# Kernel tuning notes

Hardware: AMD Instinct MI355X
Metric: run time of the kernel (lower is better)

## Reference

```python
import jax, jax.numpy as jnp
import numpy as np
from jax import lax

L, H, C, V, BLK = 6, 12, 768, 50257, 1024
B, T = 4, 1024
HD = C // H
EPS = 1e-5


def _norm(key, shape, scale=0.02):
    return jax.random.normal(key, shape, dtype=jnp.float32) * scale


def setup_inputs() -> dict:
    key = jax.random.key(0)
    ks = jax.random.split(key, 16)
    idx = jax.random.randint(ks[0], (B, T), 0, V)
    inp = {
        "idx": idx,
        "wte": _norm(ks[1], (V, C)),
        "wpe": _norm(ks[2], (BLK, C)),
        "ln1_s": jnp.ones((L, C)),
        "ln1_b": jnp.zeros((L, C)),
        "qkv_w": _norm(ks[3], (L, C, 3 * C)),
        "qkv_b": jnp.zeros((L, 3 * C)),
        "proj_w": _norm(ks[4], (L, C, C)),
        "proj_b": jnp.zeros((L, C)),
        "ln2_s": jnp.ones((L, C)),
        "ln2_b": jnp.zeros((L, C)),
        "fc_w": _norm(ks[5], (L, C, 4 * C)),
        "fc_b": jnp.zeros((L, 4 * C)),
        "fcp_w": _norm(ks[6], (L, 4 * C, C)),
        "fcp_b": jnp.zeros((L, C)),
        "lnf_s": jnp.ones((C,)),
        "lnf_b": jnp.zeros((C,)),
    }
    return inp


def layer_norm(x, s, b):
    mu = jnp.mean(x, axis=-1, keepdims=True)
    var = jnp.mean(jnp.square(x - mu), axis=-1, keepdims=True)
    return (x - mu) * lax.rsqrt(var + EPS) * s + b


def block(x, p):
    ln1_s, ln1_b, qkv_w, qkv_b, proj_w, proj_b, ln2_s, ln2_b, fc_w, fc_b, fcp_w, fcp_b = p
    Bx, Tx, Cx = x.shape
    h = layer_norm(x, ln1_s, ln1_b)
    qkv = h @ qkv_w + qkv_b  # [B,T,3C]
    q, k, v = jnp.split(qkv, 3, axis=-1)
    q = q.reshape(Bx, Tx, H, HD).swapaxes(1, 2)  # [B,H,T,hd]
    k = k.reshape(Bx, Tx, H, HD).swapaxes(1, 2)
    v = v.reshape(Bx, Tx, H, HD).swapaxes(1, 2)
    attn = jnp.einsum("bhqd,bhkd->bhqk", q, k) / jnp.sqrt(jnp.float32(HD))
    mask = jnp.tril(jnp.ones((Tx, Tx), dtype=bool))
    attn = jnp.where(mask, attn, -jnp.inf)
    attn = jax.nn.softmax(attn, axis=-1)
    y = jnp.einsum("bhqk,bhkd->bhqd", attn, v)
    y = y.swapaxes(1, 2).reshape(Bx, Tx, Cx)
    x = x + (y @ proj_w + proj_b)
    h = layer_norm(x, ln2_s, ln2_b)
    h = jax.nn.gelu(h @ fc_w + fc_b, approximate=True)
    x = x + (h @ fcp_w + fcp_b)
    return x


def reference(idx, wte, wpe, ln1_s, ln1_b, qkv_w, qkv_b, proj_w, proj_b,
              ln2_s, ln2_b, fc_w, fc_b, fcp_w, fcp_b, lnf_s, lnf_b):
    Tx = idx.shape[1]
    x = wte[idx] + wpe[:Tx][None]  # [B,T,C]
    params = (ln1_s, ln1_b, qkv_w, qkv_b, proj_w, proj_b,
              ln2_s, ln2_b, fc_w, fc_b, fcp_w, fcp_b)
    def step(carry, p):
        return block(carry, p), None
    x, _ = lax.scan(step, x, params)
    x = layer_norm(x, lnf_s, lnf_b)
    logits = x @ wte.T  # tied embedding attend
    return logits
```

## Files before the change

### kernel.cpp

```cpp
#include <hip/hip_runtime.h>
#include <math.h>

#define LNUM 6
#define HNUM 12
#define CDIM 768
#define VDIM 50257
#define BDIM 4
#define TDIM 1024
#define NTOK 4096

typedef __bf16 bf16;
typedef __bf16 bf16x8 __attribute__((ext_vector_type(8)));
typedef float  floatx4 __attribute__((ext_vector_type(4)));
typedef unsigned int u32;

__device__ inline void gload16(const bf16* gsrc, bf16* lds) {
  __builtin_amdgcn_global_load_lds(
      (const __attribute__((address_space(1))) u32*)gsrc,
      (__attribute__((address_space(3))) u32*)lds, 16, 0, 0);
}

__global__ void k_cvt_bf16(const float* __restrict__ in, bf16* __restrict__ out, long n) {
  long i = ((long)blockIdx.x * blockDim.x + threadIdx.x) * 4;
  long stride = (long)gridDim.x * blockDim.x * 4;
  for (; i < n; i += stride) {
    float4 v = *reinterpret_cast<const float4*>(in + i);
    bf16 b0 = (bf16)v.x, b1 = (bf16)v.y, b2 = (bf16)v.z, b3 = (bf16)v.w;
    ushort4 pk;
    pk.x = __builtin_bit_cast(unsigned short, b0);
    pk.y = __builtin_bit_cast(unsigned short, b1);
    pk.z = __builtin_bit_cast(unsigned short, b2);
    pk.w = __builtin_bit_cast(unsigned short, b3);
    *reinterpret_cast<ushort4*>(out + i) = pk;
  }
}

#define TILES_QKV  1728
#define TILES_PROJ 576
#define TILES_FC   2304
#define TILES_FCP  2304
#define TILES_LAYER (TILES_QKV + TILES_PROJ + TILES_FC + TILES_FCP)

__global__ __launch_bounds__(256) void k_trans_all(
    const float* __restrict__ qkv_w, const float* __restrict__ proj_w,
    const float* __restrict__ fc_w, const float* __restrict__ fcp_w,
    bf16* __restrict__ wq, bf16* __restrict__ wp,
    bf16* __restrict__ wf, bf16* __restrict__ wfp) {
  __shared__ float tile[32][33];
  int bid = blockIdx.x;
  int layer = bid / TILES_LAYER, r = bid % TILES_LAYER;
  const float* src; bf16* dst; int K, N, tx, ty;
  if (r < TILES_QKV) {
    src = qkv_w + (size_t)layer * CDIM * 3 * CDIM; dst = wq + (size_t)layer * CDIM * 3 * CDIM;
    K = CDIM; N = 3 * CDIM; tx = r % 72; ty = r / 72;
  } else if (r < TILES_QKV + TILES_PROJ) {
    r -= TILES_QKV;
    src = proj_w + (size_t)layer * CDIM * CDIM; dst = wp + (size_t)layer * CDIM * CDIM;
    K = CDIM; N = CDIM; tx = r % 24; ty = r / 24;
  } else if (r < TILES_QKV + TILES_PROJ + TILES_FC) {
    r -= TILES_QKV + TILES_PROJ;
    src = fc_w + (size_t)layer * CDIM * 4 * CDIM; dst = wf + (size_t)layer * CDIM * 4 * CDIM;
    K = CDIM; N = 4 * CDIM; tx = r % 96; ty = r / 96;
  } else {
    r -= TILES_QKV + TILES_PROJ + TILES_FC;
    src = fcp_w + (size_t)layer * 4 * CDIM * CDIM; dst = wfp + (size_t)layer * 4 * CDIM * CDIM;
    K = 4 * CDIM; N = CDIM; tx = r % 24; ty = r / 24;
  }
  int n0 = tx * 32, k0 = ty * 32;
  int nx = threadIdx.x & 31, tyy = threadIdx.x >> 5;
  #pragma unroll
  for (int p = 0; p < 4; ++p) {
    int k = tyy + p * 8;
    tile[k][nx] = src[(size_t)(k0 + k) * N + n0 + nx];
  }
  __syncthreads();
  #pragma unroll
  for (int p = 0; p < 4; ++p) {
    int n = tyy + p * 8;
    dst[(size_t)(n0 + n) * K + k0 + nx] = (bf16)tile[nx][n];
  }
}

__global__ void k_embed(const int* __restrict__ idx, const float* __restrict__ wte,
                        const float* __restrict__ wpe, float* __restrict__ x) {
  int tok = blockIdx.x;
  int t = tok & (TDIM - 1);
  int id = idx[tok];
  const float* a = wte + (size_t)id * CDIM;
  const float* p = wpe + (size_t)t * CDIM;
  float* o = x + (size_t)tok * CDIM;
  for (int c = threadIdx.x; c < CDIM; c += 256) o[c] = a[c] + p[c];
}

__global__ __launch_bounds__(256) void k_layernorm(const float* __restrict__ x,
    const float* __restrict__ sc, const float* __restrict__ bi, bf16* __restrict__ out) {
  __shared__ float red[8];
  int row = blockIdx.x;
  const float* xr = x + (size_t)row * CDIM;
  int t = threadIdx.x;
  float v0 = xr[t], v1 = xr[t + 256], v2 = xr[t + 512];
  float s = v0 + v1 + v2;
  #pragma unroll
  for (int o = 32; o > 0; o >>= 1) s += __shfl_down(s, o);
  if ((t & 63) == 0) red[t >> 6] = s;
  __syncthreads();
  float mean = (red[0] + red[1] + red[2] + red[3]) * (1.0f / CDIM);
  float d0 = v0 - mean, d1 = v1 - mean, d2 = v2 - mean;
  float q = d0 * d0 + d1 * d1 + d2 * d2;
  #pragma unroll
  for (int o = 32; o > 0; o >>= 1) q += __shfl_down(q, o);
  if ((t & 63) == 0) red[4 + (t >> 6)] = q;
  __syncthreads();
  float var = (red[4] + red[5] + red[6] + red[7]) * (1.0f / CDIM);
  float rs = rsqrtf(var + 1e-5f);
  bf16* orow = out + (size_t)row * CDIM;
  orow[t]       = (bf16)(d0 * rs * sc[t]       + bi[t]);
  orow[t + 256] = (bf16)(d1 * rs * sc[t + 256] + bi[t + 256]);
  orow[t + 512] = (bf16)(d2 * rs * sc[t + 512] + bi[t + 512]);
}

__device__ inline float gelu_f(float x) {
  float x3 = x * x * x;
  return 0.5f * x * (1.0f + tanhf(0.7978845608028654f * (x + 0.044715f * x3)));
}

__global__ __launch_bounds__(512, 1) void k_gemm_logits(
    const bf16* __restrict__ A, const bf16* __restrict__ Bt,
    float* __restrict__ Cf, int N, int K) {
  __shared__ __align__(16) bf16 smem[7 * 8192];
  bf16* Bs = smem;
  bf16* As = smem + 4 * 8192;
  const int nwg = gridDim.x;
  const int id = blockIdx.x;
  const int swz = (id & 7) * (nwg >> 3) + (id >> 3);
  const int m0 = (swz & 15) * 256;
  const int n0 = (swz >> 4) * 256;
  const int tid = threadIdx.x, lane = tid & 63, wave = tid >> 6;
  const int wr = wave >> 2, wc = wave & 3;
  const int g = lane >> 4, r16 = lane & 15;
  const int numK = K >> 5;
  const int wsl = wave * 512;

  const int srow = wave * 16 + (lane >> 2);
  const int scol = ((lane & 3) ^ ((lane >> 3) & 3)) * 8;
  const bf16* at  = A  + (size_t)(m0 + srow) * K + scol;
  const bf16* at1 = A  + (size_t)(m0 + srow + 128) * K + scol;
  const bf16* bt  = Bt + (size_t)(n0 + srow) * K + scol;
  const bf16* bt1 = Bt + (size_t)(n0 + srow + 128) * K + scol;
  const int sw = (g ^ ((r16 >> 1) & 3)) * 8;
  const int a_off = (wr * 128 + r16) * 32 + sw;
  const int b_off = (wc * 64 + r16) * 32 + sw;

  floatx4 acc[8][4] = {};

#define STBd(s0, s1, pb) do { gload16((s0), Bs + (pb) * 8192 + wsl); \
                              gload16((s1), Bs + (pb) * 8192 + wsl + 4096); } while (0)
#define STAd(s0, s1, pb) do { gload16((s0), As + (pb) * 8192 + wsl); \
                              gload16((s1), As + (pb) * 8192 + wsl + 4096); } while (0)

  STBd(bt,      bt1,      0);
  STAd(at,      at1,      0);
  STBd(bt + 32, bt1 + 32, 1);
  STAd(at + 32, at1 + 32, 1);
  STBd(bt + 64, bt1 + 64, 2);
  asm volatile("s_waitcnt vmcnt(6)" ::: "memory");
  __builtin_amdgcn_s_barrier();

  for (int t = 0; t < numK; ++t) {
    const int ab = t % 3, bb = t & 3;
    bf16x8 af[4], bfr[4];

    #pragma unroll
    for (int j = 0; j < 4; ++j) bfr[j] = *(const bf16x8*)&Bs[bb * 8192 + b_off + j * 512];
    #pragma unroll
    for (int i = 0; i < 4; ++i) af[i] = *(const bf16x8*)&As[ab * 8192 + a_off + i * 512];
    if (t + 2 < numK) STAd(at + 64, at1 + 64, (t + 2) % 3);
    __builtin_amdgcn_s_barrier();
    asm volatile("s_waitcnt lgkmcnt(0)" ::: "memory");
    __builtin_amdgcn_s_setprio(1);
    #pragma unroll
    for (int i = 0; i < 4; ++i)
      #pragma unroll
      for (int j = 0; j < 4; ++j)
        acc[i][j] = __builtin_amdgcn_mfma_f32_16x16x32_bf16(af[i], bfr[j], acc[i][j], 0, 0, 0);
    __builtin_amdgcn_s_setprio(0);
    __builtin_amdgcn_s_barrier();

    #pragma unroll
    for (int i = 0; i < 4; ++i) af[i] = *(const bf16x8*)&As[ab * 8192 + a_off + (i + 4) * 512];
    if (t + 3 < numK) STBd(bt + 96, bt1 + 96, (t + 3) & 3);
    __builtin_amdgcn_s_barrier();
    asm volatile("s_waitcnt lgkmcnt(0)" ::: "memory");
    __builtin_amdgcn_s_setprio(1);
    #pragma unroll
    for (int i = 0; i < 4; ++i)
      #pragma unroll
      for (int j = 0; j < 4; ++j)
        acc[i + 4][j] = __builtin_amdgcn_mfma_f32_16x16x32_bf16(af[i], bfr[j], acc[i + 4][j], 0, 0, 0);
    __builtin_amdgcn_s_setprio(0);
    if (t + 3 < numK)      { asm volatile("s_waitcnt vmcnt(6)" ::: "memory"); }
    else if (t + 2 < numK) { asm volatile("s_waitcnt vmcnt(4)" ::: "memory"); }
    else                   { asm volatile("s_waitcnt vmcnt(0)" ::: "memory"); }
    __builtin_amdgcn_s_barrier();

    at += 32; at1 += 32; bt += 32; bt1 += 32;
  }
#undef STBd
#undef STAd

  float* sb = reinterpret_cast<float*>(smem) + wave * 1088;
  const int seg = lane & 15, rq = lane >> 4;
  const int mrow_base = m0 + wr * 128;
  const int ncol_base = n0 + wc * 64;
  #pragma unroll
  for (int mf = 0; mf < 8; ++mf) {
    #pragma unroll
    for (int nf = 0; nf < 4; ++nf) {
      #pragma unroll
      for (int q = 0; q < 4; ++q)
        sb[(g * 4 + q) * 68 + nf * 16 + r16] = acc[mf][nf][q];
    }
    #pragma unroll
    for (int pz = 0; pz < 4; ++pz) {
      int row = rq + pz * 4;
      floatx4 v = *reinterpret_cast<const floatx4*>(&sb[row * 68 + seg * 4]);
      int m = mrow_base + mf * 16 + row;
      int n = ncol_base + seg * 4;
      if (n + 4 <= N) {
        __builtin_nontemporal_store(v, reinterpret_cast<floatx4*>(&Cf[(size_t)m * N + n]));
      } else {
        #pragma unroll
        for (int e = 0; e < 4; ++e)
          if (n + e < N) Cf[(size_t)m * N + n + e] = v[e];
      }
    }
  }
}

template<int TBM, int EPI>
__global__ __launch_bounds__(512, 1) void k_gemm8(
    const bf16* __restrict__ A, const bf16* __restrict__ Bt,
    const float* __restrict__ bias,
    float* __restrict__ Cf, bf16* __restrict__ Cb,
    int N, int K) {
  constexpr int MI = TBM / 32;
  constexpr int MH = MI / 2;
  constexpr int MTILES = 4096 / TBM;
  __shared__ __align__(16) bf16 smem[2 * 8192 + 2 * TBM * 32];
  bf16* Bs = smem;
  bf16* As = smem + 2 * 8192;
  const int nwg = gridDim.x;
  const int id = blockIdx.x;
  const int swz = (id & 7) * (nwg >> 3) + (id >> 3);
  const int m0 = (swz % MTILES) * TBM;
  const int n0 = (swz / MTILES) * 256;
  const int tid = threadIdx.x, lane = tid & 63, wave = tid >> 6;
  const int wr = wave >> 2, wc = wave & 3;
  const int g = lane >> 4, r16 = lane & 15;
  const int numK = K >> 5;
  const int wsl = wave * 512;

  const int srow = wave * 16 + (lane >> 2);
  const int scol = ((lane & 3) ^ ((lane >> 3) & 3)) * 8;
  const bf16* at  = A  + (size_t)(m0 + srow) * K + scol;
  const bf16* at1 = A  + (size_t)(m0 + srow + 128) * K + scol;
  const bf16* bt  = Bt + (size_t)(n0 + srow) * K + scol;
  const bf16* bt1 = Bt + (size_t)(n0 + srow + 128) * K + scol;
  const int sw = (g ^ ((r16 >> 1) & 3)) * 8;
  const int a_off = (wr * (TBM / 2) + r16) * 32 + sw;
  const int b_off = (wc * 64 + r16) * 32 + sw;

  floatx4 acc[MI][4] = {};

#define STB(s0, s1, pb) do { gload16((s0), Bs + (pb) * 8192 + wsl); \
                             gload16((s1), Bs + (pb) * 8192 + wsl + 4096); } while (0)
#define STA(s0, s1, pb) do { gload16((s0), As + (pb) * TBM * 32 + wsl); \
                             if constexpr (TBM == 256) gload16((s1), As + (pb) * TBM * 32 + wsl + 4096); } while (0)

  STB(bt, bt1, 0);
  STA(at, at1, 0);
  STB(bt + 32, bt1 + 32, 1);
  asm volatile("s_waitcnt vmcnt(2)" ::: "memory");
  __builtin_amdgcn_s_barrier();

  for (int t = 0; t < numK; ++t) {
    const int p = t & 1, pn = p ^ 1;
    bf16x8 af[MH], bfr[4];

    #pragma unroll
    for (int j = 0; j < 4; ++j) bfr[j] = *(const bf16x8*)&Bs[p * 8192 + b_off + j * 512];
    #pragma unroll
    for (int i = 0; i < MH; ++i) af[i] = *(const bf16x8*)&As[p * TBM * 32 + a_off + i * 512];
    if (t + 1 < numK) STA(at + 32, at1 + 32, pn);
    __builtin_amdgcn_s_barrier();
    asm volatile("s_waitcnt lgkmcnt(0)" ::: "memory");
    __builtin_amdgcn_s_setprio(1);
    #pragma unroll
    for (int i = 0; i < MH; ++i)
      #pragma unroll
      for (int j = 0; j < 4; ++j)
        acc[i][j] = __builtin_amdgcn_mfma_f32_16x16x32_bf16(af[i], bfr[j], acc[i][j], 0, 0, 0);
    __builtin_amdgcn_s_setprio(0);
    __builtin_amdgcn_s_barrier();

    #pragma unroll
    for (int i = 0; i < MH; ++i) af[i] = *(const bf16x8*)&As[p * TBM * 32 + a_off + (i + MH) * 512];
    if (t + 2 < numK) STB(bt + 64, bt1 + 64, p);
    __builtin_amdgcn_s_barrier();
    asm volatile("s_waitcnt lgkmcnt(0)" ::: "memory");
    __builtin_amdgcn_s_setprio(1);
    #pragma unroll
    for (int i = 0; i < MH; ++i)
      #pragma unroll
      for (int j = 0; j < 4; ++j)
        acc[i + MH][j] = __builtin_amdgcn_mfma_f32_16x16x32_bf16(af[i], bfr[j], acc[i + MH][j], 0, 0, 0);
    __builtin_amdgcn_s_setprio(0);
    if (t + 2 < numK) { asm volatile("s_waitcnt vmcnt(2)" ::: "memory"); }
    else              { asm volatile("s_waitcnt vmcnt(0)" ::: "memory"); }
    __builtin_amdgcn_s_barrier();

    at += 32; at1 += 32; bt += 32; bt1 += 32;
  }
#undef STB
#undef STA

  bf16* sb = smem + wave * 1152;
  const int rr_rd = lane & 15, seg = lane >> 4;
  const int nb = n0 + wc * 64 + r16;
  float bv[4];
  #pragma unroll
  for (int j = 0; j < 4; ++j) bv[j] = bias[nb + j * 16];
  #pragma unroll
  for (int mf = 0; mf < MI; ++mf) {
    #pragma unroll
    for (int j = 0; j < 4; ++j) {
      #pragma unroll
      for (int q = 0; q < 4; ++q) {
        float v = acc[mf][j][q] + bv[j];
        if (EPI == 3) v = gelu_f(v);
        sb[(g * 4 + q) * 72 + j * 16 + r16] = (bf16)v;
      }
    }
    bf16x8 o0 = *(const bf16x8*)&sb[rr_rd * 72 + seg * 16];
    bf16x8 o1 = *(const bf16x8*)&sb[rr_rd * 72 + seg * 16 + 8];
    size_t orow = (size_t)(m0 + wr * (TBM / 2) + mf * 16 + rr_rd) * N + (n0 + wc * 64 + seg * 16);
    *(bf16x8*)&Cb[orow] = o0;
    *(bf16x8*)&Cb[orow + 8] = o1;
  }
}

template<int TBM, int MI, int NI, int EPI>
__global__ __launch_bounds__(256) void k_gemm(
    const bf16* __restrict__ A, const bf16* __restrict__ Bt,
    const float* __restrict__ bias, const float* __restrict__ resid,
    float* __restrict__ Cf, bf16* __restrict__ Cb,
    int M, int N, int K) {
  constexpr int BN = 128;
  constexpr int WGN = BN / (NI * 16);
  constexpr int AI = TBM / 32;
  constexpr int BI = BN / 32;
  __shared__ __align__(16) bf16 As[TBM * 64];
  __shared__ __align__(16) bf16 Bs[BN * 64];
  const int m0 = blockIdx.x * TBM, n0 = blockIdx.y * BN;
  const int tid = threadIdx.x;
  const int lane = tid & 63, wave = tid >> 6;
  const int wr = wave / WGN, wc = wave % WGN;
  const int l8 = lane >> 3, s8 = lane & 7;
  const int g = lane >> 4, r16 = lane & 15;

  floatx4 acc[MI][NI] = {};

  const bf16* a_src = A + (size_t)(m0 + l8) * K + s8 * 8;
  const bf16* b_src = Bt + (size_t)(n0 + l8) * K + s8 * 8;

  for (int k0 = 0; k0 < K; k0 += 64) {
    #pragma unroll
    for (int t = 0; t < AI; ++t) {
      int row0 = wave * (TBM / 4) + t * 8;
      gload16(a_src + (size_t)row0 * K + k0, &As[row0 * 64]);
    }
    #pragma unroll
    for (int t = 0; t < BI; ++t) {
      int row0 = wave * 32 + t * 8;
      gload16(b_src + (size_t)row0 * K + k0, &Bs[row0 * 64]);
    }
    __syncthreads();
    #pragma unroll
    for (int kk = 0; kk < 2; ++kk) {
      bf16x8 af[MI], bfr[NI];
      #pragma unroll
      for (int i = 0; i < MI; ++i)
        af[i] = *reinterpret_cast<const bf16x8*>(&As[(wr * MI * 16 + i * 16 + r16) * 64 + g * 8 + kk * 32]);
      #pragma unroll
      for (int j = 0; j < NI; ++j)
        bfr[j] = *reinterpret_cast<const bf16x8*>(&Bs[(wc * NI * 16 + j * 16 + r16) * 64 + g * 8 + kk * 32]);
      #pragma unroll
      for (int i = 0; i < MI; ++i) {
        #pragma unroll
        for (int j = 0; j < NI; ++j)
          acc[i][j] = __builtin_amdgcn_mfma_f32_16x16x32_bf16(af[i], bfr[j], acc[i][j], 0, 0, 0);
      }
    }
    __syncthreads();
  }

  int mb = m0 + wr * MI * 16 + g * 4;
  int nb = n0 + wc * NI * 16 + r16;
  #pragma unroll
  for (int j = 0; j < NI; ++j) {
    int n = nb + j * 16;
    if (n >= N) continue;
    float bv = (EPI >= 2) ? bias[n] : 0.0f;
    #pragma unroll
    for (int i = 0; i < MI; ++i) {
      #pragma unroll
      for (int q = 0; q < 4; ++q) {
        int m = mb + i * 16 + q;
        float v = acc[i][j][q] + bv;
        size_t o = (size_t)m * N + n;
        if (EPI == 2)      Cf[o] = v + resid[o];
        else if (EPI == 3) Cb[o] = (bf16)gelu_f(v);
        else if (EPI == 4) Cb[o] = (bf16)v;
        else               Cf[o] = v;
      }
    }
  }
}

__global__ __launch_bounds__(256) void k_vtrans(const bf16* __restrict__ qkv, bf16* __restrict__ vt) {
  __shared__ bf16 tile[64][72];
  int bh = blockIdx.x, t0 = blockIdx.y * 64;
  int b = bh / HNUM, h = bh % HNUM;
  int tid = threadIdx.x;
  int r8 = tid >> 3, s8 = tid & 7;
  #pragma unroll
  for (int p = 0; p < 2; ++p) {
    int row = p * 32 + r8;
    uint4 v = *reinterpret_cast<const uint4*>(
        qkv + (size_t)(b * TDIM + t0 + row) * (3 * CDIM) + 2 * CDIM + h * 64 + s8 * 8);
    *reinterpret_cast<uint4*>(&tile[row][s8 * 8]) = v;
  }
  __syncthreads();
  int d = tid >> 2, q4 = tid & 3;
  #pragma unroll
  for (int half = 0; half < 2; ++half) {
    int t = q4 * 16 + half * 8;
    bf16x8 o;
    #pragma unroll
    for (int u = 0; u < 8; ++u) o[u] = tile[t + u][d];
    *reinterpret_cast<bf16x8*>(vt + (size_t)bh * (64 * TDIM) + (size_t)d * TDIM + t0 + t) = o;
  }
}

__global__ __launch_bounds__(256) void k_attn(const bf16* __restrict__ qkv,
                                              const bf16* __restrict__ vt,
                                              bf16* __restrict__ y) {
  __shared__ __align__(16) bf16 Ks[64 * 64];
  __shared__ __align__(16) bf16 Vs[64 * 64];
  __shared__ __align__(16) bf16 Ps[64 * 64];
  const int bh = blockIdx.x, qt = blockIdx.y;
  const int b = bh / HNUM, h = bh % HNUM;
  const int tid = threadIdx.x, lane = tid & 63, wave = tid >> 6;
  const int g = lane >> 4, r16 = lane & 15;
  const int w16 = wave * 16;
  const int r8 = tid >> 3, s8 = tid & 7;

  bf16x8 qf[2];
  {
    const bf16* qsrc = qkv + (size_t)(b * TDIM + qt * 64 + w16 + r16) * (3 * CDIM) + h * 64 + g * 8;
    qf[0] = *reinterpret_cast<const bf16x8*>(qsrc);
    qf[1] = *reinterpret_cast<const bf16x8*>(qsrc + 32);
  }

  float m_r[4], l_r[4];
  floatx4 yacc[4] = {};
  #pragma unroll
  for (int q = 0; q < 4; ++q) { m_r[q] = -1e30f; l_r[q] = 0.f; }

  for (int kt = 0; kt <= qt; ++kt) {
    __syncthreads();
    #pragma unroll
    for (int p = 0; p < 2; ++p) {
      int row = p * 32 + r8;
      uint4 kv = *reinterpret_cast<const uint4*>(
          qkv + (size_t)(b * TDIM + kt * 64 + row) * (3 * CDIM) + CDIM + h * 64 + s8 * 8);
      *reinterpret_cast<uint4*>(&Ks[row * 64 + ((s8 ^ (row & 7)) * 8)]) = kv;
      uint4 vv = *reinterpret_cast<const uint4*>(
          vt + (size_t)bh * (64 * TDIM) + (size_t)row * TDIM + kt * 64 + s8 * 8);
      *reinterpret_cast<uint4*>(&Vs[row * 64 + ((s8 ^ (row & 7)) * 8)]) = vv;
    }
    __syncthreads();

    floatx4 sa[4] = {};
    #pragma unroll
    for (int c = 0; c < 2; ++c) {
      bf16x8 kf[4];
      #pragma unroll
      for (int j = 0; j < 4; ++j) {
        int krow = j * 16 + r16;
        kf[j] = *reinterpret_cast<const bf16x8*>(&Ks[krow * 64 + (((g + 4 * c) ^ (krow & 7)) * 8)]);
      }
      #pragma unroll
      for (int j = 0; j < 4; ++j)
        sa[j] = __builtin_amdgcn_mfma_f32_16x16x32_bf16(qf[c], kf[j], sa[j], 0, 0, 0);
    }

    const bool diag = (kt == qt);
    float p_v[4][4];
    #pragma unroll
    for (int q = 0; q < 4; ++q) {
      int qrow = w16 + g * 4 + q;
      float mx = -1e30f;
      #pragma unroll
      for (int j = 0; j < 4; ++j) {
        float s = sa[j][q] * 0.125f;
        if (diag && (r16 + j * 16) > qrow) s = -1e30f;
        p_v[j][q] = s;
        mx = fmaxf(mx, s);
      }
      #pragma unroll
      for (int o = 1; o < 16; o <<= 1) mx = fmaxf(mx, __shfl_xor(mx, o));
      float mnew = fmaxf(m_r[q], mx);
      float ps = 0.f;
      #pragma unroll
      for (int j = 0; j < 4; ++j) {
        float p = __expf(p_v[j][q] - mnew);
        p_v[j][q] = p;
        ps += p;
      }
      #pragma unroll
      for (int o = 1; o < 16; o <<= 1) ps += __shfl_xor(ps, o);
      float alpha = __expf(m_r[q] - mnew);
      m_r[q] = mnew;
      l_r[q] = l_r[q] * alpha + ps;
      #pragma unroll
      for (int j = 0; j < 4; ++j) yacc[j][q] *= alpha;
      #pragma unroll
      for (int j = 0; j < 4; ++j) {
        int col = r16 + j * 16;
        Ps[qrow * 64 + (col ^ ((qrow & 7) << 3))] = (bf16)p_v[j][q];
      }
    }

    #pragma unroll
    for (int ks = 0; ks < 2; ++ks) {
      int prow = w16 + r16;
      bf16x8 pa = *reinterpret_cast<const bf16x8*>(&Ps[prow * 64 + (((g + 4 * ks) ^ (prow & 7)) * 8)]);
      #pragma unroll
      for (int j = 0; j < 4; ++j) {
        int vrow = j * 16 + r16;
        bf16x8 vb = *reinterpret_cast<const bf16x8*>(&Vs[vrow * 64 + (((g + 4 * ks) ^ (vrow & 7)) * 8)]);
        yacc[j] = __builtin_amdgcn_mfma_f32_16x16x32_bf16(pa, vb, yacc[j], 0, 0, 0);
      }
    }
  }

  #pragma unroll
  for (int q = 0; q < 4; ++q) {
    float inv = 1.0f / l_r[q];
    int tok = b * TDIM + qt * 64 + w16 + g * 4 + q;
    #pragma unroll
    for (int j = 0; j < 4; ++j)
      y[(size_t)tok * CDIM + h * 64 + r16 + j * 16] = (bf16)(yacc[j][q] * inv);
  }
}

extern "C" void kernel_launch(void* const* d_in, const int* in_sizes, int n_in,
                              void* d_out, int out_size, void* d_ws, size_t ws_size,
                              hipStream_t stream) {
  (void)in_sizes; (void)n_in; (void)out_size;
  const int*   idx    = (const int*)  d_in[0];
  const float* wte    = (const float*)d_in[1];
  const float* wpe    = (const float*)d_in[2];
  const float* ln1_s  = (const float*)d_in[3];
  const float* ln1_b  = (const float*)d_in[4];
  const float* qkv_w  = (const float*)d_in[5];
  const float* qkv_b  = (const float*)d_in[6];
  const float* proj_w = (const float*)d_in[7];
  const float* proj_b = (const float*)d_in[8];
  const float* ln2_s  = (const float*)d_in[9];
  const float* ln2_b  = (const float*)d_in[10];
  const float* fc_w   = (const float*)d_in[11];
  const float* fc_b   = (const float*)d_in[12];
  const float* fcp_w  = (const float*)d_in[13];
  const float* fcp_b  = (const float*)d_in[14];
  const float* lnf_s  = (const float*)d_in[15];
  const float* lnf_b  = (const float*)d_in[16];
  float* logits = (float*)d_out;

  char* base = (char*)d_ws;
  size_t off = 0;
  auto alloc = [&](size_t bytes) -> void* {
    void* p = base + off;
    off += (bytes + 255) & ~(size_t)255;
    return p;
  };
  bf16*  wte_bf  = (bf16*) alloc((size_t)VDIM * CDIM * 2);
  bf16*  wq_all  = (bf16*) alloc((size_t)LNUM * 3 * CDIM * CDIM * 2);
  bf16*  wp_all  = (bf16*) alloc((size_t)LNUM * CDIM * CDIM * 2);
  bf16*  wf_all  = (bf16*) alloc((size_t)LNUM * 4 * CDIM * CDIM * 2);
  bf16*  wfp_all = (bf16*) alloc((size_t)LNUM * 4 * CDIM * CDIM * 2);
  float* x       = (float*)alloc((size_t)NTOK * CDIM * 4);
  bf16*  hb      = (bf16*) alloc((size_t)NTOK * CDIM * 2);
  bf16*  qkv_bf  = (bf16*) alloc((size_t)NTOK * 3 * CDIM * 2);
  bf16*  vt      = (bf16*) alloc((size_t)BDIM * HNUM * 64 * TDIM * 2);
  bf16*  yb      = (bf16*) alloc((size_t)NTOK * CDIM * 2);
  bf16*  gb      = (bf16*) alloc((size_t)NTOK * 4 * CDIM * 2);
  if (off > ws_size) return;

  k_cvt_bf16<<<4096, 256, 0, stream>>>(wte, wte_bf, (long)VDIM * CDIM);
  k_trans_all<<<LNUM * TILES_LAYER, 256, 0, stream>>>(qkv_w, proj_w, fc_w, fcp_w,
                                                      wq_all, wp_all, wf_all, wfp_all);
  k_embed<<<NTOK, 256, 0, stream>>>(idx, wte, wpe, x);

  for (int l = 0; l < LNUM; ++l) {
    const bf16* wq  = wq_all  + (size_t)l * 3 * CDIM * CDIM;
    const bf16* wp  = wp_all  + (size_t)l * CDIM * CDIM;
    const bf16* wf  = wf_all  + (size_t)l * 4 * CDIM * CDIM;
    const bf16* wfp = wfp_all + (size_t)l * 4 * CDIM * CDIM;

    k_layernorm<<<NTOK, 256, 0, stream>>>(x, ln1_s + l*CDIM, ln1_b + l*CDIM, hb);
    k_gemm8<128,4><<<32 * 9, 512, 0, stream>>>(hb, wq, qkv_b + (size_t)l*3*CDIM, nullptr, qkv_bf, 3*CDIM, CDIM);
    k_vtrans<<<dim3(BDIM*HNUM, TDIM/64), 256, 0, stream>>>(qkv_bf, vt);
    k_attn<<<dim3(BDIM*HNUM, TDIM/64), 256, 0, stream>>>(qkv_bf, vt, yb);
    k_gemm<64,4,2,2><<<dim3(NTOK/64, 6), 256, 0, stream>>>(yb, wp, proj_b + (size_t)l*CDIM, x, x, nullptr, NTOK, CDIM, CDIM);
    k_layernorm<<<NTOK, 256, 0, stream>>>(x, ln2_s + l*CDIM, ln2_b + l*CDIM, hb);
    k_gemm8<128,3><<<32 * 12, 512, 0, stream>>>(hb, wf, fc_b + (size_t)l*4*CDIM, nullptr, gb, 4*CDIM, CDIM);
    k_gemm<64,4,2,2><<<dim3(NTOK/64, 6), 256, 0, stream>>>(gb, wfp, fcp_b + (size_t)l*CDIM, x, x, nullptr, NTOK, CDIM, 4*CDIM);
  }

  k_layernorm<<<NTOK, 256, 0, stream>>>(x, lnf_s, lnf_b, hb);
  int ntile = (VDIM + 255) / 256;
  k_gemm_logits<<<16 * ntile, 512, 0, stream>>>(hb, wte_bf, logits, VDIM, CDIM);
}
```

Before: 1.827 ms.

## Pipeline projection GEMMs with double-buffered LDS and widen attention tiles to 128 queries

Replaces the generic 64x128 projection/FC-proj GEMM with a 128x128 kernel that double-buffers A and B tiles in swizzled LDS, splits each K-step into two MFMA phases with barriers and priority hints, and adds an XCD-aware block swizzle. Attention now handles 128 query rows per block with 8 waves sharing each K/V tile, so K/V loads are amortized over more queries, and waves past the causal limit skip compute. The logits store also changes from a nontemporal store to a plain memcpy store. The cost is fewer workgroups (192 for the projections) and some idle waves on diagonal attention tiles.

```diff
diff --git a/kernel.cpp b/kernel.cpp
--- a/kernel.cpp
+++ b/kernel.cpp
@@ -227,7 +227,7 @@
       int m = mrow_base + mf * 16 + row;
       int n = ncol_base + seg * 4;
       if (n + 4 <= N) {
-        __builtin_nontemporal_store(v, reinterpret_cast<floatx4*>(&Cf[(size_t)m * N + n]));
+        __builtin_memcpy(&Cf[(size_t)m * N + n], &v, 16);
       } else {
         #pragma unroll
         for (int e = 0; e < 4; ++e)
@@ -349,79 +349,101 @@
   }
 }
 
-template<int TBM, int MI, int NI, int EPI>
-__global__ __launch_bounds__(256) void k_gemm(
+__global__ __launch_bounds__(256, 1) void k_gemmp(
     const bf16* __restrict__ A, const bf16* __restrict__ Bt,
-    const float* __restrict__ bias, const float* __restrict__ resid,
-    float* __restrict__ Cf, bf16* __restrict__ Cb,
-    int M, int N, int K) {
-  constexpr int BN = 128;
-  constexpr int WGN = BN / (NI * 16);
-  constexpr int AI = TBM / 32;
-  constexpr int BI = BN / 32;
-  __shared__ __align__(16) bf16 As[TBM * 64];
-  __shared__ __align__(16) bf16 Bs[BN * 64];
-  const int m0 = blockIdx.x * TBM, n0 = blockIdx.y * BN;
-  const int tid = threadIdx.x;
-  const int lane = tid & 63, wave = tid >> 6;
-  const int wr = wave / WGN, wc = wave % WGN;
-  const int l8 = lane >> 3, s8 = lane & 7;
+    const float* __restrict__ bias, float* __restrict__ Cf,
+    int N, int K) {
+  __shared__ __align__(16) bf16 smem[4 * 4096];
+  bf16* Bs = smem;
+  bf16* As = smem + 2 * 4096;
+  const int nwg = gridDim.x;
+  const int id = blockIdx.x;
+  const int swz = (id & 7) * (nwg >> 3) + (id >> 3);
+  const int m0 = (swz & 31) * 128;
+  const int n0 = (swz >> 5) * 128;
+  const int tid = threadIdx.x, lane = tid & 63, wave = tid >> 6;
+  const int wr = wave >> 1, wc = wave & 1;
   const int g = lane >> 4, r16 = lane & 15;
-
-  floatx4 acc[MI][NI] = {};
-
-  const bf16* a_src = A + (size_t)(m0 + l8) * K + s8 * 8;
-  const bf16* b_src = Bt + (size_t)(n0 + l8) * K + s8 * 8;
-
-  for (int k0 = 0; k0 < K; k0 += 64) {
-    #pragma unroll
-    for (int t = 0; t < AI; ++t) {
-      int row0 = wave * (TBM / 4) + t * 8;
-      gload16(a_src + (size_t)row0 * K + k0, &As[row0 * 64]);
-    }
-    #pragma unroll
-    for (int t = 0; t < BI; ++t) {
-      int row0 = wave * 32 + t * 8;
-      gload16(b_src + (size_t)row0 * K + k0, &Bs[row0 * 64]);
-    }
-    __syncthreads();
-    #pragma unroll
-    for (int kk = 0; kk < 2; ++kk) {
-      bf16x8 af[MI], bfr[NI];
-      #pragma unroll
-      for (int i = 0; i < MI; ++i)
-        af[i] = *reinterpret_cast<const bf16x8*>(&As[(wr * MI * 16 + i * 16 + r16) * 64 + g * 8 + kk * 32]);
-      #pragma unroll
-      for (int j = 0; j < NI; ++j)
-        bfr[j] = *reinterpret_cast<const bf16x8*>(&Bs[(wc * NI * 16 + j * 16 + r16) * 64 + g * 8 + kk * 32]);
-      #pragma unroll
-      for (int i = 0; i < MI; ++i) {
-        #pragma unroll
-        for (int j = 0; j < NI; ++j)
-          acc[i][j] = __builtin_amdgcn_mfma_f32_16x16x32_bf16(af[i], bfr[j], acc[i][j], 0, 0, 0);
-      }
-    }
-    __syncthreads();
-  }
-
-  int mb = m0 + wr * MI * 16 + g * 4;
-  int nb = n0 + wc * NI * 16 + r16;
-  #pragma unroll
-  for (int j = 0; j < NI; ++j) {
+  const int numK = K >> 5;
+  const int wsl = wave * 512;
+
+  const int srow = wave * 16 + (lane >> 2);
+  const int scol = ((lane & 3) ^ ((lane >> 3) & 3)) * 8;
+  const bf16* at  = A  + (size_t)(m0 + srow) * K + scol;
+  const bf16* at1 = A  + (size_t)(m0 + srow + 64) * K + scol;
+  const bf16* bt  = Bt + (size_t)(n0 + srow) * K + scol;
+  const bf16* bt1 = Bt + (size_t)(n0 + srow + 64) * K + scol;
+  const int sw = (g ^ ((r16 >> 1) & 3)) * 8;
+  const int a_off = (wr * 64 + r16) * 32 + sw;
+  const int b_off = (wc * 64 + r16) * 32 + sw;
+
+  floatx4 acc[4][4] = {};
+
+#define STBp(s0, s1, pb) do { gload16((s0), Bs + (pb) * 4096 + wsl); \
+                              gload16((s1), Bs + (pb) * 4096 + 2048 + wsl); } while (0)
+#define STAp(s0, s1, pb) do { gload16((s0), As + (pb) * 4096 + wsl); \
+                              gload16((s1), As + (pb) * 4096 + 2048 + wsl); } while (0)
+
+  STBp(bt, bt1, 0);
+  STAp(at, at1, 0);
+  STBp(bt + 32, bt1 + 32, 1);
+  asm volatile("s_waitcnt vmcnt(2)" ::: "memory");
+  __builtin_amdgcn_s_barrier();
+
+  for (int t = 0; t < numK; ++t) {
+    const int p = t & 1, pn = p ^ 1;
+    bf16x8 af[2], bfr[4];
+
+    #pragma unroll
+    for (int j = 0; j < 4; ++j) bfr[j] = *(const bf16x8*)&Bs[p * 4096 + b_off + j * 512];
+    #pragma unroll
+    for (int i = 0; i < 2; ++i) af[i] = *(const bf16x8*)&As[p * 4096 + a_off + i * 512];
+    if (t + 1 < numK) STAp(at + 32, at1 + 32, pn);
+    __builtin_amdgcn_s_barrier();
+    asm volatile("s_waitcnt lgkmcnt(0)" ::: "memory");
+    __builtin_amdgcn_s_setprio(1);
+    #pragma unroll
+    for (int i = 0; i < 2; ++i)
+      #pragma unroll
+      for (int j = 0; j < 4; ++j)
+        acc[i][j] = __builtin_amdgcn_mfma_f32_16x16x32_bf16(af[i], bfr[j], acc[i][j], 0, 0, 0);
+    __builtin_amdgcn_s_setprio(0);
+    __builtin_amdgcn_s_barrier();
+
+    #pragma unroll
+    for (int i = 0; i < 2; ++i) af[i] = *(const bf16x8*)&As[p * 4096 + a_off + (i + 2) * 512];
+    if (t + 2 < numK) STBp(bt + 64, bt1 + 64, p);
+    __builtin_amdgcn_s_barrier();
+    asm volatile("s_waitcnt lgkmcnt(0)" ::: "memory");
+    __builtin_amdgcn_s_setprio(1);
+    #pragma unroll
+    for (int i = 0; i < 2; ++i)
+      #pragma unroll
+      for (int j = 0; j < 4; ++j)
+        acc[i + 2][j] = __builtin_amdgcn_mfma_f32_16x16x32_bf16(af[i], bfr[j], acc[i + 2][j], 0, 0, 0);
+    __builtin_amdgcn_s_setprio(0);
+    if (t + 2 < numK) { asm volatile("s_waitcnt vmcnt(2)" ::: "memory"); }
+    else              { asm volatile("s_waitcnt vmcnt(0)" ::: "memory"); }
+    __builtin_amdgcn_s_barrier();
+
+    at += 32; at1 += 32; bt += 32; bt1 += 32;
+  }
+#undef STBp
+#undef STAp
+
+  const int mb = m0 + wr * 64 + g * 4;
+  const int nb = n0 + wc * 64 + r16;
+  #pragma unroll
+  for (int j = 0; j < 4; ++j) {
     int n = nb + j * 16;
-    if (n >= N) continue;
-    float bv = (EPI >= 2) ? bias[n] : 0.0f;
-    #pragma unroll
-    for (int i = 0; i < MI; ++i) {
+    float bv = bias[n];
+    #pragma unroll
+    for (int i = 0; i < 4; ++i) {
       #pragma unroll
       for (int q = 0; q < 4; ++q) {
         int m = mb + i * 16 + q;
-        float v = acc[i][j][q] + bv;
         size_t o = (size_t)m * N + n;
-        if (EPI == 2)      Cf[o] = v + resid[o];
-        else if (EPI == 3) Cb[o] = (bf16)gelu_f(v);
-        else if (EPI == 4) Cb[o] = (bf16)v;
-        else               Cf[o] = v;
+        Cf[o] = Cf[o] + acc[i][j][q] + bv;
       }
     }
   }
@@ -452,22 +474,23 @@
   }
 }
 
-__global__ __launch_bounds__(256) void k_attn(const bf16* __restrict__ qkv,
+__global__ __launch_bounds__(512) void k_attn(const bf16* __restrict__ qkv,
                                               const bf16* __restrict__ vt,
                                               bf16* __restrict__ y) {
   __shared__ __align__(16) bf16 Ks[64 * 64];
   __shared__ __align__(16) bf16 Vs[64 * 64];
-  __shared__ __align__(16) bf16 Ps[64 * 64];
+  __shared__ __align__(16) bf16 Ps[128 * 64];
   const int bh = blockIdx.x, qt = blockIdx.y;
   const int b = bh / HNUM, h = bh % HNUM;
   const int tid = threadIdx.x, lane = tid & 63, wave = tid >> 6;
   const int g = lane >> 4, r16 = lane & 15;
   const int w16 = wave * 16;
+  const int qtb = qt * 128;
   const int r8 = tid >> 3, s8 = tid & 7;
 
   bf16x8 qf[2];
   {
-    const bf16* qsrc = qkv + (size_t)(b * TDIM + qt * 64 + w16 + r16) * (3 * CDIM) + h * 64 + g * 8;
+    const bf16* qsrc = qkv + (size_t)(b * TDIM + qtb + w16 + r16) * (3 * CDIM) + h * 64 + g * 8;
     qf[0] = *reinterpret_cast<const bf16x8*>(qsrc);
     qf[1] = *reinterpret_cast<const bf16x8*>(qsrc + 32);
   }
@@ -477,11 +500,13 @@
   #pragma unroll
   for (int q = 0; q < 4; ++q) { m_r[q] = -1e30f; l_r[q] = 0.f; }
 
-  for (int kt = 0; kt <= qt; ++kt) {
+  const int ktmax = 2 * qt + 1;
+  const int wave_qmax = qtb + w16 + 15;
+
+  for (int kt = 0; kt <= ktmax; ++kt) {
     __syncthreads();
-    #pragma unroll
-    for (int p = 0; p < 2; ++p) {
-      int row = p * 32 + r8;
+    {
+      int row = r8;
       uint4 kv = *reinterpret_cast<const uint4*>(
           qkv + (size_t)(b * TDIM + kt * 64 + row) * (3 * CDIM) + CDIM + h * 64 + s8 * 8);
       *reinterpret_cast<uint4*>(&Ks[row * 64 + ((s8 ^ (row & 7)) * 8)]) = kv;
@@ -490,6 +515,7 @@
       *reinterpret_cast<uint4*>(&Vs[row * 64 + ((s8 ^ (row & 7)) * 8)]) = vv;
     }
     __syncthreads();
+    if (kt * 64 > wave_qmax) continue;
 
     floatx4 sa[4] = {};
     #pragma unroll
@@ -505,16 +531,17 @@
         sa[j] = __builtin_amdgcn_mfma_f32_16x16x32_bf16(qf[c], kf[j], sa[j], 0, 0, 0);
     }
 
-    const bool diag = (kt == qt);
+    const int kbase = kt * 64;
     float p_v[4][4];
     #pragma unroll
     for (int q = 0; q < 4; ++q) {
-      int qrow = w16 + g * 4 + q;
+      int qrl = w16 + g * 4 + q;
+      int qrow = qtb + qrl;
       float mx = -1e30f;
       #pragma unroll
       for (int j = 0; j < 4; ++j) {
         float s = sa[j][q] * 0.125f;
-        if (diag && (r16 + j * 16) > qrow) s = -1e30f;
+        if (kbase + r16 + j * 16 > qrow) s = -1e30f;
         p_v[j][q] = s;
         mx = fmaxf(mx, s);
       }
@@ -538,7 +565,7 @@
       #pragma unroll
       for (int j = 0; j < 4; ++j) {
         int col = r16 + j * 16;
-        Ps[qrow * 64 + (col ^ ((qrow & 7) << 3))] = (bf16)p_v[j][q];
+        Ps[qrl * 64 + (col ^ ((qrl & 7) << 3))] = (bf16)p_v[j][q];
       }
     }
 
@@ -558,7 +585,7 @@
   #pragma unroll
   for (int q = 0; q < 4; ++q) {
     float inv = 1.0f / l_r[q];
-    int tok = b * TDIM + qt * 64 + w16 + g * 4 + q;
+    int tok = b * TDIM + qtb + w16 + g * 4 + q;
     #pragma unroll
     for (int j = 0; j < 4; ++j)
       y[(size_t)tok * CDIM + h * 64 + r16 + j * 16] = (bf16)(yacc[j][q] * inv);
@@ -622,11 +649,11 @@
     k_layernorm<<<NTOK, 256, 0, stream>>>(x, ln1_s + l*CDIM, ln1_b + l*CDIM, hb);
     k_gemm8<128,4><<<32 * 9, 512, 0, stream>>>(hb, wq, qkv_b + (size_t)l*3*CDIM, nullptr, qkv_bf, 3*CDIM, CDIM);
     k_vtrans<<<dim3(BDIM*HNUM, TDIM/64), 256, 0, stream>>>(qkv_bf, vt);
-    k_attn<<<dim3(BDIM*HNUM, TDIM/64), 256, 0, stream>>>(qkv_bf, vt, yb);
-    k_gemm<64,4,2,2><<<dim3(NTOK/64, 6), 256, 0, stream>>>(yb, wp, proj_b + (size_t)l*CDIM, x, x, nullptr, NTOK, CDIM, CDIM);
+    k_attn<<<dim3(BDIM*HNUM, TDIM/128), 512, 0, stream>>>(qkv_bf, vt, yb);
+    k_gemmp<<<32 * 6, 256, 0, stream>>>(yb, wp, proj_b + (size_t)l*CDIM, x, CDIM, CDIM);
     k_layernorm<<<NTOK, 256, 0, stream>>>(x, ln2_s + l*CDIM, ln2_b + l*CDIM, hb);
     k_gemm8<128,3><<<32 * 12, 512, 0, stream>>>(hb, wf, fc_b + (size_t)l*4*CDIM, nullptr, gb, 4*CDIM, CDIM);
-    k_gemm<64,4,2,2><<<dim3(NTOK/64, 6), 256, 0, stream>>>(gb, wfp, fcp_b + (size_t)l*CDIM, x, x, nullptr, NTOK, CDIM, 4*CDIM);
+    k_gemmp<<<32 * 6, 256, 0, stream>>>(gb, wfp, fcp_b + (size_t)l*CDIM, x, CDIM, 4*CDIM);
   }
 
   k_layernorm<<<NTOK, 256, 0, stream>>>(x, lnf_s, lnf_b, hb);
```

After: 1.882 ms. +3.0%, slower.
